# Optimization experiments

Measured on AMD Instinct MI355X. Metric: run time of the kernel, lower is better.

## Reference

```python
import jax, jax.numpy as jnp
import numpy as np

B, SQ, SK, D, DV = 16, 2048, 2048, 64, 64
DROPOUT_P = 0.1


def setup_inputs() -> dict:
    key = jax.random.key(0)
    k1, k2, k3, k4 = jax.random.split(key, 4)
    return {
        "query": jax.random.normal(k1, (B, SQ, D), dtype=jnp.float32),
        "key": jax.random.normal(k2, (B, SK, D), dtype=jnp.float32),
        "value": jax.random.normal(k3, (B, SK, DV), dtype=jnp.float32),
        "drop_mask": jax.random.uniform(k4, (B, SQ, SK), dtype=jnp.float32),
    }


def reference(query, key, value, drop_mask):
    # scaled dot-product attention with explicit score matrix, as in the module
    scale = jnp.sqrt(jnp.asarray(key.shape[-1], dtype=query.dtype))
    qk = jnp.einsum("bqd,bkd->bqk", query, key) / scale  # [B, SQ, SK]
    attn = jax.nn.softmax(qk, axis=-1)
    # dropout: keep where uniform > p, rescale by 1/(1-p)
    keep = (drop_mask > DROPOUT_P).astype(attn.dtype)
    attn = attn * keep / (1.0 - DROPOUT_P)
    return jnp.einsum("bqk,bkv->bqv", attn, value)  # [B, SQ, DV]
```

## Files before the change

kernel.cpp:

```cpp
#include <hip/hip_runtime.h>
#include <hip/hip_bf16.h>

#define B_ 16
#define SQ_ 2048
#define SK_ 2048
#define D_ 64
#define DV_ 64
#define INV_KEEP 1.1111111f

typedef float f4 __attribute__((ext_vector_type(4)));
typedef __bf16 bf16x2 __attribute__((ext_vector_type(2)));
typedef __bf16 bf16x8 __attribute__((ext_vector_type(8)));
typedef short s16x4 __attribute__((ext_vector_type(4)));
typedef unsigned int u32;
typedef unsigned int u32x2 __attribute__((ext_vector_type(2)));
typedef unsigned int u32x4 __attribute__((ext_vector_type(4)));

static __device__ __forceinline__ unsigned short bf16u(float f) {
    u32 u = __builtin_bit_cast(u32, f);
    u += 0x7fffu + ((u >> 16) & 1u);
    return (unsigned short)(u >> 16);
}
static __device__ __forceinline__ u32 pk2(float lo, float hi) {
    return (u32)bf16u(lo) | ((u32)bf16u(hi) << 16);
}
static __device__ __forceinline__ u32 pkc(float lo, float hi) {
    bf16x2 t = {(__bf16)lo, (__bf16)hi};
    return __builtin_bit_cast(u32, t);
}

static __device__ __forceinline__ void gload16(const void* g, void* l) {
    __builtin_amdgcn_global_load_lds(
        (const __attribute__((address_space(1))) unsigned int*)g,
        (__attribute__((address_space(3))) unsigned int*)l, 16, 0, 0);
}

template <int OFF>
static __device__ __forceinline__ f4 gload_f4(const float* p) {
    f4 d;
    if constexpr (OFF == 0)
        asm volatile("global_load_dwordx4 %0, %1, off" : "=v"(d) : "v"(p));
    else
        asm volatile("global_load_dwordx4 %0, %1, off offset:%2" : "=v"(d) : "v"(p), "i"(OFF));
    return d;
}

static __device__ __forceinline__ f4 mfma16(s16x4 a, s16x4 b, f4 c) {
#if __has_builtin(__builtin_amdgcn_mfma_f32_16x16x16bf16_1k)
    return __builtin_amdgcn_mfma_f32_16x16x16bf16_1k(a, b, c, 0, 0, 0);
#else
    f4 d;
    asm("v_mfma_f32_16x16x16_bf16 %0, %1, %2, %3" : "=v"(d) : "v"(a), "v"(b), "v"(c));
    return d;
#endif
}

__global__ __launch_bounds__(256) void k_retile(const float* __restrict__ K,
                                                unsigned short* __restrict__ KbT) {
    int b = blockIdx.x >> 6, kt = blockIdx.x & 63;
    int p = threadIdx.x;
    int s = p >> 6, g = (p >> 4) & 3, c = p & 15;
    int t = s & 1, h = s >> 1;
    const float* src = K + ((size_t)(b * SK_ + kt * 32 + 16 * t + c)) * D_ + 32 * h + 8 * g;
    f4 a = *(const f4*)src;
    f4 b2 = *(const f4*)(src + 4);
    u32x4 w;
    w[0] = pk2(a.x, a.y); w[1] = pk2(a.z, a.w);
    w[2] = pk2(b2.x, b2.y); w[3] = pk2(b2.z, b2.w);
    *(u32x4*)(KbT + ((size_t)(b * 64 + kt)) * 2048 + (size_t)p * 8) = w;
}

__global__ __launch_bounds__(256) void v_retile(const float* __restrict__ V,
                                                unsigned short* __restrict__ VtT) {
    __shared__ float vt[32][65];
    int b = blockIdx.x >> 6, kt = blockIdx.x & 63;
    int tid = threadIdx.x;
#pragma unroll
    for (int e = 0; e < 2; ++e) {
        int f = tid * 2 + e;
        int row = f >> 4, c4 = (f & 15) * 4;
        *(f4*)&vt[row][c4] = *(const f4*)(V + ((size_t)(b * SK_ + kt * 32 + row)) * DV_ + c4);
    }
    __syncthreads();
    int vb = tid >> 6, g = (tid >> 4) & 3, c = tid & 15;
    int v = vb * 16 + c;
    u32x4 w;
    w[0] = pk2(vt[4 * g + 0][v], vt[4 * g + 1][v]);
    w[1] = pk2(vt[4 * g + 2][v], vt[4 * g + 3][v]);
    w[2] = pk2(vt[16 + 4 * g + 0][v], vt[16 + 4 * g + 1][v]);
    w[3] = pk2(vt[16 + 4 * g + 2][v], vt[16 + 4 * g + 3][v]);
    *(u32x4*)(VtT + ((size_t)(b * 64 + kt)) * 2048 + (size_t)tid * 8) = w;
}

template <int SPLIT>
__global__ __launch_bounds__(256) void attn_main(const float* __restrict__ Q,
                                                 const unsigned short* __restrict__ KbT,
                                                 const unsigned short* __restrict__ VtT,
                                                 const float* __restrict__ mask,
                                                 float* __restrict__ out,
                                                 float* __restrict__ accP,
                                                 float* __restrict__ lP) {
    constexpr int NT32 = SK_ / SPLIT / 32;
    constexpr int NB = 512 * SPLIT;
    __shared__ unsigned short sK[4][2048];
    __shared__ unsigned short sV[4][2048];

    int bswz = (blockIdx.x & 7) * (NB / 8) + (blockIdx.x >> 3);
    int wid  = threadIdx.x >> 6;
    int split = bswz & (SPLIT - 1);
    int strip = (bswz / SPLIT) * 4 + wid;
    int b  = strip >> 7;
    int q0 = (strip & 127) << 4;
    int kb = split * (SK_ / SPLIT);
    int lane = threadIdx.x & 63;
    int g = lane >> 4, c = lane & 15;

    const size_t tile0 = ((size_t)b * 64 + split * NT32) * 2048;
    const unsigned short* ksrc = KbT + tile0 + (size_t)threadIdx.x * 8;
    const unsigned short* vsrc = VtT + tile0 + (size_t)threadIdx.x * 8;
    const float* msrc = mask + ((size_t)(b * SQ_ + q0 + c)) * SK_ + kb + 4 * g;

    bf16x8 qf[2];
    {
        const float* qp = Q + ((size_t)(b * SQ_ + q0 + c)) * D_ + 8 * g;
#pragma unroll
        for (int h = 0; h < 2; ++h) {
            f4 a  = *(const f4*)(qp + h * 32);
            f4 bq = *(const f4*)(qp + h * 32 + 4);
            u32x4 wq;
            wq[0] = pk2(a.x * 0.125f, a.y * 0.125f);
            wq[1] = pk2(a.z * 0.125f, a.w * 0.125f);
            wq[2] = pk2(bq.x * 0.125f, bq.y * 0.125f);
            wq[3] = pk2(bq.z * 0.125f, bq.w * 0.125f);
            qf[h] = __builtin_bit_cast(bf16x8, wq);
        }
    }

    f4 mreg[4][2];

    auto stage = [&](int dst, int srct) {
        gload16(ksrc + (size_t)srct * 2048, &sK[dst][wid * 512]);
        gload16(vsrc + (size_t)srct * 2048, &sV[dst][wid * 512]);
        const float* mp = msrc + (size_t)srct * 32;
        mreg[dst][0] = gload_f4<0>(mp);
        mreg[dst][1] = gload_f4<64>(mp);
    };

    stage(0, 0);
    stage(1, 1);
    stage(2, 2);

    f4 acc[4];
#pragma unroll
    for (int vb = 0; vb < 4; ++vb) acc[vb] = (f4){0.f, 0.f, 0.f, 0.f};
    f4 ls0 = (f4){0.f, 0.f, 0.f, 0.f}, ls1 = (f4){0.f, 0.f, 0.f, 0.f};

    const unsigned short* kbL = &sK[0][0] + lane * 8;
    const unsigned short* vbL = &sV[0][0] + lane * 8;

#pragma unroll 4
    for (int kt = 0; kt < NT32; ++kt) {
        asm volatile("s_waitcnt vmcnt(8)" ::: "memory");
        __builtin_amdgcn_s_barrier();
        __builtin_amdgcn_sched_barrier(0);

        const int bi = kt & 3;
        const unsigned short* kB = kbL + bi * 2048;
        const unsigned short* vB = vbL + bi * 2048;

        u32x4 ka0 = *(const u32x4*)(kB);
        u32x4 ka1 = *(const u32x4*)(kB + 1024);
        u32x4 kc0 = *(const u32x4*)(kB + 512);
        u32x4 kc1 = *(const u32x4*)(kB + 1536);
        f4 st0 = (f4){0.f, 0.f, 0.f, 0.f}, st1 = (f4){0.f, 0.f, 0.f, 0.f};
        st0 = __builtin_amdgcn_mfma_f32_16x16x32_bf16(__builtin_bit_cast(bf16x8, ka0), qf[0], st0, 0, 0, 0);
        st0 = __builtin_amdgcn_mfma_f32_16x16x32_bf16(__builtin_bit_cast(bf16x8, ka1), qf[1], st0, 0, 0, 0);
        st1 = __builtin_amdgcn_mfma_f32_16x16x32_bf16(__builtin_bit_cast(bf16x8, kc0), qf[0], st1, 0, 0, 0);
        st1 = __builtin_amdgcn_mfma_f32_16x16x32_bf16(__builtin_bit_cast(bf16x8, kc1), qf[1], st1, 0, 0, 0);

        const f4 mk0 = mreg[bi][0], mk1 = mreg[bi][1];
        float pd0[4], pd1[4];
#pragma unroll
        for (int r = 0; r < 4; ++r) {
            float p0 = __expf(st0[r]);
            ls0[r] += p0;
            pd0[r] = (mk0[r] > 0.1f) ? p0 : 0.f;
            float p1 = __expf(st1[r]);
            ls1[r] += p1;
            pd1[r] = (mk1[r] > 0.1f) ? p1 : 0.f;
        }

        u32x2 pw0, pw1;
        pw0[0] = pkc(pd0[0], pd0[1]); pw0[1] = pkc(pd0[2], pd0[3]);
        pw1[0] = pkc(pd1[0], pd1[1]); pw1[1] = pkc(pd1[2], pd1[3]);
        s16x4 pb0 = __builtin_bit_cast(s16x4, pw0);
        s16x4 pb1 = __builtin_bit_cast(s16x4, pw1);
#pragma unroll
        for (int vb = 0; vb < 4; ++vb) {
            u32x4 vv = *(const u32x4*)(vB + vb * 512);
            u32x2 vlo, vhi;
            vlo[0] = vv[0]; vlo[1] = vv[1];
            vhi[0] = vv[2]; vhi[1] = vv[3];
            acc[vb] = mfma16(__builtin_bit_cast(s16x4, vlo), pb0, acc[vb]);
            acc[vb] = mfma16(__builtin_bit_cast(s16x4, vhi), pb1, acc[vb]);
        }

        __builtin_amdgcn_s_barrier();
        stage((kt + 3) & 3, (kt + 3 < NT32) ? (kt + 3) : (NT32 - 1));
    }
    asm volatile("s_waitcnt vmcnt(0)" ::: "memory");

    float lf = ls0[0] + ls0[1] + ls0[2] + ls0[3] + ls1[0] + ls1[1] + ls1[2] + ls1[3];
    lf += __shfl_xor(lf, 16);
    lf += __shfl_xor(lf, 32);

    if constexpr (SPLIT == 1) {
        float li = INV_KEEP / lf;
        float* op = out + ((size_t)(b * SQ_ + q0 + c)) * DV_;
#pragma unroll
        for (int vb = 0; vb < 4; ++vb) {
            f4 o = acc[vb] * li;
            __builtin_nontemporal_store(o, (f4*)(op + 16 * vb + 4 * g));
        }
    } else {
        float* ap = accP + (((size_t)strip * SPLIT + split) * 64 + lane) * 16;
#pragma unroll
        for (int vb = 0; vb < 4; ++vb)
            *(f4*)(ap + 4 * vb) = acc[vb];
        if (g == 0)
            lP[((size_t)strip * SPLIT + split) * 16 + c] = lf;
    }
}

__global__ __launch_bounds__(256) void attn_combine2(const float* __restrict__ accP,
                                                     const float* __restrict__ lP,
                                                     float* __restrict__ out) {
    __shared__ float sacc[2 * 1280];
    __shared__ float sl[32];
    int strip = blockIdx.x;
    int t = threadIdx.x;
    const float* src = accP + (size_t)strip * 2048;
#pragma unroll
    for (int s = 0; s < 2; ++s)
        *(f4*)&sacc[s * 1280 + (t >> 2) * 20 + (t & 3) * 4] = *(const f4*)(src + s * 1024 + t * 4);
    if (t < 32) sl[t] = lP[(size_t)strip * 32 + t];
    __syncthreads();

    int q = t >> 4, j = t & 15;
    float L = sl[q] + sl[16 + q];
    float inv = INV_KEEP / L;
    int base = (16 * (j & 3) + q) * 20 + 4 * (j >> 2);
    f4 o = *(const f4*)&sacc[base] + *(const f4*)&sacc[1280 + base];
    o *= inv;
    int b  = strip >> 7;
    int q0 = (strip & 127) << 4;
    __builtin_nontemporal_store(o, (f4*)(out + ((size_t)(b * SQ_ + q0 + q)) * DV_ + 4 * j));
}

extern "C" void kernel_launch(void* const* d_in, const int* in_sizes, int n_in,
                              void* d_out, int out_size, void* d_ws, size_t ws_size,
                              hipStream_t stream) {
    const float* Q = (const float*)d_in[0];
    const float* K = (const float*)d_in[1];
    const float* V = (const float*)d_in[2];
    const float* M = (const float*)d_in[3];
    float* out = (float*)d_out;

    char* ws = (char*)d_ws;
    unsigned short* KbT  = (unsigned short*)ws;
    unsigned short* VtT  = (unsigned short*)(ws + (size_t)4 * 1024 * 1024);
    float*          accP = (float*)         (ws + (size_t)8 * 1024 * 1024);
    float*          lP   = (float*)         (ws + (size_t)24 * 1024 * 1024);

    const size_t need_split = (size_t)24 * 1024 * 1024 + (size_t)2048 * 2 * 16 * 4;

    k_retile<<<1024, 256, 0, stream>>>(K, KbT);
    v_retile<<<1024, 256, 0, stream>>>(V, VtT);
    if (ws_size >= need_split) {
        attn_main<2><<<1024, 256, 0, stream>>>(Q, KbT, VtT, M, out, accP, lP);
        attn_combine2<<<2048, 256, 0, stream>>>(accP, lP, out);
    } else {
        attn_main<1><<<512, 256, 0, stream>>>(Q, KbT, VtT, M, out, nullptr, nullptr);
    }
}
```

Baseline: 95.56 us.

## Prefetch dropout mask one tile deeper, use exp2, and merge K/V retile kernels

The staging lambda is split so the dropout-mask register loads run four tiles ahead while the K/V LDS loads stay three tiles ahead. The vmcnt wait threshold is adjusted to match the new issue order. The softmax exponent now uses the hardware exp2, with log2(e)/sqrt(D) folded into the Q pre-scale. The separate K and V retile kernels are combined into one launch. The aim is to hide more latency on the mask stream, which dominates memory traffic, and to save some ALU work and one kernel launch. In exchange, more mask loads are in flight per wave and the wait counts are tighter to get right.

```diff
diff --git a/kernel.cpp b/kernel.cpp
--- a/kernel.cpp
+++ b/kernel.cpp
@@ -7,6 +7,7 @@
 #define D_ 64
 #define DV_ 64
 #define INV_KEEP 1.1111111f
+#define QSCALE 0.1803368801f
 
 typedef float f4 __attribute__((ext_vector_type(4)));
 typedef __bf16 bf16x2 __attribute__((ext_vector_type(2)));
@@ -27,6 +28,14 @@
 static __device__ __forceinline__ u32 pkc(float lo, float hi) {
     bf16x2 t = {(__bf16)lo, (__bf16)hi};
     return __builtin_bit_cast(u32, t);
+}
+
+static __device__ __forceinline__ float fexp2(float x) {
+#if __has_builtin(__builtin_amdgcn_exp2f)
+    return __builtin_amdgcn_exp2f(x);
+#else
+    return exp2f(x);
+#endif
 }
 
 static __device__ __forceinline__ void gload16(const void* g, void* l) {
@@ -55,41 +64,43 @@
 #endif
 }
 
-__global__ __launch_bounds__(256) void k_retile(const float* __restrict__ K,
-                                                unsigned short* __restrict__ KbT) {
-    int b = blockIdx.x >> 6, kt = blockIdx.x & 63;
-    int p = threadIdx.x;
-    int s = p >> 6, g = (p >> 4) & 3, c = p & 15;
-    int t = s & 1, h = s >> 1;
-    const float* src = K + ((size_t)(b * SK_ + kt * 32 + 16 * t + c)) * D_ + 32 * h + 8 * g;
-    f4 a = *(const f4*)src;
-    f4 b2 = *(const f4*)(src + 4);
-    u32x4 w;
-    w[0] = pk2(a.x, a.y); w[1] = pk2(a.z, a.w);
-    w[2] = pk2(b2.x, b2.y); w[3] = pk2(b2.z, b2.w);
-    *(u32x4*)(KbT + ((size_t)(b * 64 + kt)) * 2048 + (size_t)p * 8) = w;
-}
-
-__global__ __launch_bounds__(256) void v_retile(const float* __restrict__ V,
-                                                unsigned short* __restrict__ VtT) {
-    __shared__ float vt[32][65];
-    int b = blockIdx.x >> 6, kt = blockIdx.x & 63;
-    int tid = threadIdx.x;
-#pragma unroll
-    for (int e = 0; e < 2; ++e) {
-        int f = tid * 2 + e;
-        int row = f >> 4, c4 = (f & 15) * 4;
-        *(f4*)&vt[row][c4] = *(const f4*)(V + ((size_t)(b * SK_ + kt * 32 + row)) * DV_ + c4);
-    }
-    __syncthreads();
-    int vb = tid >> 6, g = (tid >> 4) & 3, c = tid & 15;
-    int v = vb * 16 + c;
-    u32x4 w;
-    w[0] = pk2(vt[4 * g + 0][v], vt[4 * g + 1][v]);
-    w[1] = pk2(vt[4 * g + 2][v], vt[4 * g + 3][v]);
-    w[2] = pk2(vt[16 + 4 * g + 0][v], vt[16 + 4 * g + 1][v]);
-    w[3] = pk2(vt[16 + 4 * g + 2][v], vt[16 + 4 * g + 3][v]);
-    *(u32x4*)(VtT + ((size_t)(b * 64 + kt)) * 2048 + (size_t)tid * 8) = w;
+__global__ __launch_bounds__(256) void kv_retile(const float* __restrict__ K,
+                                                 const float* __restrict__ V,
+                                                 unsigned short* __restrict__ KbT,
+                                                 unsigned short* __restrict__ VtT) {
+    if (blockIdx.x < 1024) {
+        int b = blockIdx.x >> 6, kt = blockIdx.x & 63;
+        int p = threadIdx.x;
+        int s = p >> 6, g = (p >> 4) & 3, c = p & 15;
+        int t = s & 1, h = s >> 1;
+        const float* src = K + ((size_t)(b * SK_ + kt * 32 + 16 * t + c)) * D_ + 32 * h + 8 * g;
+        f4 a = *(const f4*)src;
+        f4 b2 = *(const f4*)(src + 4);
+        u32x4 w;
+        w[0] = pk2(a.x, a.y); w[1] = pk2(a.z, a.w);
+        w[2] = pk2(b2.x, b2.y); w[3] = pk2(b2.z, b2.w);
+        *(u32x4*)(KbT + ((size_t)(b * 64 + kt)) * 2048 + (size_t)p * 8) = w;
+    } else {
+        __shared__ float vt[32][65];
+        int id = blockIdx.x - 1024;
+        int b = id >> 6, kt = id & 63;
+        int tid = threadIdx.x;
+#pragma unroll
+        for (int e = 0; e < 2; ++e) {
+            int f = tid * 2 + e;
+            int row = f >> 4, c4 = (f & 15) * 4;
+            *(f4*)&vt[row][c4] = *(const f4*)(V + ((size_t)(b * SK_ + kt * 32 + row)) * DV_ + c4);
+        }
+        __syncthreads();
+        int vb = tid >> 6, g = (tid >> 4) & 3, c = tid & 15;
+        int v = vb * 16 + c;
+        u32x4 w;
+        w[0] = pk2(vt[4 * g + 0][v], vt[4 * g + 1][v]);
+        w[1] = pk2(vt[4 * g + 2][v], vt[4 * g + 3][v]);
+        w[2] = pk2(vt[16 + 4 * g + 0][v], vt[16 + 4 * g + 1][v]);
+        w[3] = pk2(vt[16 + 4 * g + 2][v], vt[16 + 4 * g + 3][v]);
+        *(u32x4*)(VtT + ((size_t)(b * 64 + kt)) * 2048 + (size_t)tid * 8) = w;
+    }
 }
 
 template <int SPLIT>
@@ -128,27 +139,30 @@
             f4 a  = *(const f4*)(qp + h * 32);
             f4 bq = *(const f4*)(qp + h * 32 + 4);
             u32x4 wq;
-            wq[0] = pk2(a.x * 0.125f, a.y * 0.125f);
-            wq[1] = pk2(a.z * 0.125f, a.w * 0.125f);
-            wq[2] = pk2(bq.x * 0.125f, bq.y * 0.125f);
-            wq[3] = pk2(bq.z * 0.125f, bq.w * 0.125f);
+            wq[0] = pk2(a.x * QSCALE, a.y * QSCALE);
+            wq[1] = pk2(a.z * QSCALE, a.w * QSCALE);
+            wq[2] = pk2(bq.x * QSCALE, bq.y * QSCALE);
+            wq[3] = pk2(bq.z * QSCALE, bq.w * QSCALE);
             qf[h] = __builtin_bit_cast(bf16x8, wq);
         }
     }
 
     f4 mreg[4][2];
 
-    auto stage = [&](int dst, int srct) {
+    auto kvload = [&](int dst, int srct) {
         gload16(ksrc + (size_t)srct * 2048, &sK[dst][wid * 512]);
         gload16(vsrc + (size_t)srct * 2048, &sV[dst][wid * 512]);
+    };
+    auto mload = [&](int dst, int srct) {
         const float* mp = msrc + (size_t)srct * 32;
         mreg[dst][0] = gload_f4<0>(mp);
         mreg[dst][1] = gload_f4<64>(mp);
     };
 
-    stage(0, 0);
-    stage(1, 1);
-    stage(2, 2);
+    mload(0, 0);
+    kvload(0, 0); mload(1, 1);
+    kvload(1, 1); mload(2, 2);
+    kvload(2, 2); mload(3, 3);
 
     f4 acc[4];
 #pragma unroll
@@ -160,7 +174,7 @@
 
 #pragma unroll 4
     for (int kt = 0; kt < NT32; ++kt) {
-        asm volatile("s_waitcnt vmcnt(8)" ::: "memory");
+        asm volatile("s_waitcnt vmcnt(10)" ::: "memory");
         __builtin_amdgcn_s_barrier();
         __builtin_amdgcn_sched_barrier(0);
 
@@ -182,10 +196,10 @@
         float pd0[4], pd1[4];
 #pragma unroll
         for (int r = 0; r < 4; ++r) {
-            float p0 = __expf(st0[r]);
+            float p0 = fexp2(st0[r]);
             ls0[r] += p0;
             pd0[r] = (mk0[r] > 0.1f) ? p0 : 0.f;
-            float p1 = __expf(st1[r]);
+            float p1 = fexp2(st1[r]);
             ls1[r] += p1;
             pd1[r] = (mk1[r] > 0.1f) ? p1 : 0.f;
         }
@@ -206,7 +220,8 @@
         }
 
         __builtin_amdgcn_s_barrier();
-        stage((kt + 3) & 3, (kt + 3 < NT32) ? (kt + 3) : (NT32 - 1));
+        kvload((kt + 3) & 3, (kt + 3 < NT32) ? kt + 3 : NT32 - 1);
+        mload((kt + 4) & 3, (kt + 4 < NT32) ? kt + 4 : NT32 - 1);
     }
     asm volatile("s_waitcnt vmcnt(0)" ::: "memory");
 
@@ -274,8 +289,7 @@
 
     const size_t need_split = (size_t)24 * 1024 * 1024 + (size_t)2048 * 2 * 16 * 4;
 
-    k_retile<<<1024, 256, 0, stream>>>(K, KbT);
-    v_retile<<<1024, 256, 0, stream>>>(V, VtT);
+    kv_retile<<<2048, 256, 0, stream>>>(K, V, KbT, VtT);
     if (ws_size >= need_split) {
         attn_main<2><<<1024, 256, 0, stream>>>(Q, KbT, VtT, M, out, accP, lP);
         attn_combine2<<<2048, 256, 0, stream>>>(accP, lP, out);
```

Result: faster. 91.25 us (-4.5%).
